# Optimization experiments

Measured on AMD Instinct MI355X. Metric: run time of the kernel, lower is better.

Reference implementation:

```python
import jax, jax.numpy as jnp
import numpy as np

NUM_HEADS = 12
HEAD_DIM = 64
HIDDEN = NUM_HEADS * HEAD_DIM


def setup_inputs() -> dict:
    key = jax.random.key(0)
    ks = jax.random.split(key, 10)
    B, S, N_ROT = 8, 1374, 1369
    s = 0.02
    return {
        "hidden_states": jax.random.normal(ks[0], (B, S, HIDDEN), jnp.float32),
        "sin": jax.random.normal(ks[1], (N_ROT, HEAD_DIM), jnp.float32),
        "cos": jax.random.normal(ks[2], (N_ROT, HEAD_DIM), jnp.float32),
        "Wq": jax.random.normal(ks[3], (HIDDEN, HIDDEN), jnp.float32) * s,
        "bq": jax.random.normal(ks[4], (HIDDEN,), jnp.float32) * s,
        "Wk": jax.random.normal(ks[5], (HIDDEN, HIDDEN), jnp.float32) * s,
        "Wv": jax.random.normal(ks[6], (HIDDEN, HIDDEN), jnp.float32) * s,
        "bv": jax.random.normal(ks[7], (HIDDEN,), jnp.float32) * s,
        "Wp": jax.random.normal(ks[8], (HIDDEN, HIDDEN), jnp.float32) * s,
        "bp": jax.random.normal(ks[9], (HIDDEN,), jnp.float32) * s,
    }


def _rotate_half(x):
    x1, x2 = jnp.split(x, 2, axis=-1)
    return jnp.concatenate([-x2, x1], axis=-1)


def _rope_apply(x, sin, cos):
    return x * cos + _rotate_half(x) * sin


def reference(hidden_states, sin, cos, Wq, bq, Wk, Wv, bv, Wp, bp):
    B, S, _ = hidden_states.shape
    scaling = HEAD_DIM ** -0.5

    def to_heads(x):  # [B,S,HIDDEN] -> [B,H,S,D]
        return x.reshape(B, S, NUM_HEADS, HEAD_DIM).transpose(0, 2, 1, 3)

    q = to_heads(hidden_states @ Wq.T + bq)
    k = to_heads(hidden_states @ Wk.T)  # no key bias (mask_k_bias)
    v = to_heads(hidden_states @ Wv.T + bv)

    # RoPE only on patch tokens (prefix = cls + register tokens untouched)
    prefix = S - sin.shape[-2]
    q = jnp.concatenate([q[:, :, :prefix], _rope_apply(q[:, :, prefix:], sin, cos)], axis=2)
    k = jnp.concatenate([k[:, :, :prefix], _rope_apply(k[:, :, prefix:], sin, cos)], axis=2)

    # eager attention: softmax in float32, no mask, no dropout (eval)
    scores = jnp.einsum("bhqd,bhkd->bhqk", q, k) * scaling
    probs = jax.nn.softmax(scores.astype(jnp.float32), axis=-1).astype(q.dtype)
    ctx = jnp.einsum("bhqk,bhkd->bqhd", probs, v).reshape(B, S, HIDDEN)
    return ctx @ Wp.T + bp
```

## Files before the change

### kernel.cpp

```cpp
#include <hip/hip_runtime.h>
#include <stdint.h>

typedef unsigned short u16;
typedef unsigned int u32;
typedef u16 u16x8 __attribute__((ext_vector_type(8)));
typedef __bf16 bf16x8 __attribute__((ext_vector_type(8)));
typedef float f32x4 __attribute__((ext_vector_type(4)));

#define S_LEN 1374
#define S_PAD 1408
#define PRE_TOK 5
#define HID 768
#define NH 12
#define MPAD 11008

__device__ __forceinline__ u16 f2bf(float f) {
    union { float f; u32 u; } v; v.f = f;
    u32 r = v.u + 0x7fffu + ((v.u >> 16) & 1u);
    return (u16)(r >> 16);
}
__device__ __forceinline__ bf16x8 as_bf(u16x8 v) { bf16x8 r; __builtin_memcpy(&r, &v, 16); return r; }
__device__ __forceinline__ bf16x8 lds_load8(const u16* p) {
    u16x8 t = *(const u16x8*)p;
    return as_bf(t);
}
__device__ __forceinline__ u32 cvtpk_bf16(float lo, float hi) {
    u32 r;
    asm("v_cvt_pk_bf16_f32 %0, %1, %2" : "=v"(r) : "v"(lo), "v"(hi));
    return r;
}
__device__ __forceinline__ float fexp2(float x) {
    float r;
    asm("v_exp_f32 %0, %1" : "=v"(r) : "v"(x));
    return r;
}
__device__ __forceinline__ void gload16(void* lds, const void* g) {
    unsigned int __attribute__((address_space(1)))* gp =
        (unsigned int __attribute__((address_space(1)))*)(unsigned long long)g;
    unsigned int __attribute__((address_space(3)))* lp =
        (unsigned int __attribute__((address_space(3)))*)(unsigned int)(unsigned long long)lds;
    __builtin_amdgcn_global_load_lds(gp, lp, 16, 0, 0);
}
__device__ __forceinline__ int xcd_swz(int orig, int nwg) {
    int qd = nwg >> 3, rd = nwg & 7;
    int xcd = orig & 7, rem = orig >> 3;
    return (xcd < rd ? xcd * (qd + 1) : rd * (qd + 1) + (xcd - rd) * qd) + rem;
}


__global__ __launch_bounds__(256) void pack_x(const float* __restrict__ X, u16* __restrict__ Xb) {
    size_t i = (size_t)blockIdx.x * 256 + threadIdx.x;
    size_t e = i * 8;
    const size_t TOT = (size_t)10992 * HID;
    u16x8 o = {0,0,0,0,0,0,0,0};
    if (e < TOT) {
        f32x4 a = *(const f32x4*)(X + e);
        f32x4 b = *(const f32x4*)(X + e + 4);
#pragma unroll
        for (int j = 0; j < 4; ++j) { o[j] = f2bf(a[j]); o[4 + j] = f2bf(b[j]); }
    }
    *(u16x8*)(Xb + e) = o;
}

__global__ __launch_bounds__(256) void pack_w(
    const float* __restrict__ Wq, const float* __restrict__ Wk, const float* __restrict__ Wv,
    const float* __restrict__ Wp, const float* __restrict__ bq, const float* __restrict__ bv,
    u16* __restrict__ wqkv, u16* __restrict__ wpb, float* __restrict__ bqkv)
{
    int g = blockIdx.x * 256 + threadIdx.x;
    const int QKV8 = 2304 * HID / 8;
    const int P8 = HID * HID / 8;
    if (g < QKV8) {
        int e = g * 8;
        int row = e / HID, col = e - row * HID;
        const float* src = (row < 768) ? (Wq + (size_t)row * HID + col)
                         : (row < 1536) ? (Wk + (size_t)(row - 768) * HID + col)
                                        : (Wv + (size_t)(row - 1536) * HID + col);
        u16x8 o;
#pragma unroll
        for (int j = 0; j < 8; ++j) o[j] = f2bf(src[j]);
        *(u16x8*)(wqkv + e) = o;
    } else if (g < QKV8 + P8) {
        int e = (g - QKV8) * 8;
        u16x8 o;
#pragma unroll
        for (int j = 0; j < 8; ++j) o[j] = f2bf(Wp[e + j]);
        *(u16x8*)(wpb + e) = o;
    }
    if (g < 288) {
        int e = g * 8;
#pragma unroll
        for (int j = 0; j < 8; ++j) {
            int c = e + j;
            bqkv[c] = (c < 768) ? bq[c] : (c < 1536 ? 0.f : bv[c - 1536]);
        }
    }
}


template <int EPI>
__global__ __launch_bounds__(256) void gemm_nt(
    const u16* __restrict__ A, const u16* __restrict__ B, const float* __restrict__ bias,
    float* __restrict__ Yf, u16* __restrict__ Qh, u16* __restrict__ Kh,
    u16* __restrict__ Yv, const float* __restrict__ SN, const float* __restrict__ CS,
    int N, int K, int nx, int nwg)
{
    __shared__ u16 As[128 * 64];
    __shared__ u16 Bs[128 * 64];
    int tid = threadIdx.x;
    int w = tid >> 6, l = tid & 63;
    int fr = l & 15, fg = l >> 4;
    int wg = xcd_swz(blockIdx.x, nwg);
    int col0 = (wg % nx) * 128;
    int row0 = (wg / nx) * 128;
    int wr = (w >> 1) * 64, wc = (w & 1) * 64;

    f32x4 zero4 = {0.f, 0.f, 0.f, 0.f};
    f32x4 acc[4][4];
#pragma unroll
    for (int m = 0; m < 4; ++m)
#pragma unroll
        for (int n = 0; n < 4; ++n) acc[m][n] = zero4;

    int srow[4], soff[4];
#pragma unroll
    for (int i = 0; i < 4; ++i) {
        int sbyte = (i * 4 + w) * 1024 + l * 16;
        int r = sbyte >> 7;
        int ir = (sbyte & 127) ^ ((r & 7) << 4);
        srow[i] = r; soff[i] = ir >> 1;
    }

    for (int kt = 0; kt < K; kt += 64) {
#pragma unroll
        for (int i = 0; i < 4; ++i) {
            int sb = (i * 4 + w) * 1024;
            gload16((char*)As + sb, A + (size_t)(row0 + srow[i]) * K + kt + soff[i]);
            gload16((char*)Bs + sb, B + (size_t)(col0 + srow[i]) * K + kt + soff[i]);
        }
        __syncthreads();
#pragma unroll
        for (int c = 0; c < 2; ++c) {
            bf16x8 af[4], bfr[4];
#pragma unroll
            for (int m = 0; m < 4; ++m) {
                int r = wr + m * 16 + fr;
                int byte_ = (c * 64 + fg * 16) ^ ((r & 7) << 4);
                af[m] = lds_load8(As + r * 64 + (byte_ >> 1));
            }
#pragma unroll
            for (int n = 0; n < 4; ++n) {
                int r = wc + n * 16 + fr;
                int byte_ = (c * 64 + fg * 16) ^ ((r & 7) << 4);
                bfr[n] = lds_load8(Bs + r * 64 + (byte_ >> 1));
            }
#pragma unroll
            for (int m = 0; m < 4; ++m)
#pragma unroll
                for (int n = 0; n < 4; ++n)
                    acc[m][n] = __builtin_amdgcn_mfma_f32_16x16x32_bf16(af[m], bfr[n], acc[m][n], 0, 0, 0);
        }
        __syncthreads();
    }

    if (EPI == 1) {
#pragma unroll
        for (int m = 0; m < 4; ++m)
#pragma unroll
            for (int n = 0; n < 4; ++n) {
                int gn = col0 + wc + n * 16 + fr;
                float bvv = bias[gn];
#pragma unroll
                for (int j = 0; j < 4; ++j) {
                    int gm = row0 + wr + m * 16 + fg * 4 + j;
                    if (gm < 10992) Yf[(size_t)gm * N + gn] = acc[m][n][j] + bvv;
                }
            }
    } else {
        int sect = col0 >= 1536 ? 2 : (col0 >= 768 ? 1 : 0);
        if (sect == 2) {
#pragma unroll
            for (int m = 0; m < 4; ++m)
#pragma unroll
                for (int n = 0; n < 4; ++n) {
                    int gn = col0 + wc + n * 16 + fr;
                    float bvv = bias[gn];
#pragma unroll
                    for (int j = 0; j < 4; ++j) {
                        int gm = row0 + wr + m * 16 + fg * 4 + j;
                        if (gm < 10992)
                            Yv[(size_t)gm * HID + (gn - 1536)] = f2bf(acc[m][n][j] + bvv);
                    }
                }
        } else {
            u16* H = sect ? Kh : Qh;
            const float QS = sect ? 1.f : 0.125f * 1.44269504088896f;
            int hh = ((col0 + wc) >> 6) - sect * NH;
            float bv4[4];
#pragma unroll
            for (int n = 0; n < 4; ++n) bv4[n] = bias[col0 + wc + n * 16 + fr];
#pragma unroll
            for (int m = 0; m < 4; ++m)
#pragma unroll
                for (int j = 0; j < 4; ++j) {
                    int gm = row0 + wr + m * 16 + fg * 4 + j;
                    if (gm < 10992) {
                        int b = gm / 1374, s = gm - b * 1374;
                        size_t ob = ((size_t)(b * NH + hh) * S_PAD + s) * 64;
#pragma unroll
                        for (int n2 = 0; n2 < 2; ++n2) {
                            int d = n2 * 16 + fr;
                            float v1 = acc[m][n2][j] + bv4[n2];
                            float v2 = acc[m][n2 + 2][j] + bv4[n2 + 2];
                            float a1 = v1, a2 = v2;
                            if (s >= PRE_TOK) {
                                size_t rr = (size_t)(s - PRE_TOK) * 64;
                                float c1 = CS[rr + d], s1 = SN[rr + d];
                                float c2 = CS[rr + d + 32], s2 = SN[rr + d + 32];
                                a1 = v1 * c1 - v2 * s1;
                                a2 = v2 * c2 + v1 * s2;
                            }
                            H[ob + d]      = f2bf(a1 * QS);
                            H[ob + d + 32] = f2bf(a2 * QS);
                        }
                    }
                }
        }
    }
}


__global__ __launch_bounds__(256) void v_pack(const u16* __restrict__ Yv, u16* __restrict__ Vt) {
    int st = blockIdx.x, bh = blockIdx.y;
    int b = bh / NH, h = bh - b * NH;
    int tid = threadIdx.x;
    int sl = tid >> 2, dg = (tid & 3) * 8;
    int s = st * 64 + sl;
    __shared__ u16 vtile[64 * 64];

    u16x8 a = {0,0,0,0,0,0,0,0}, a2 = {0,0,0,0,0,0,0,0};
    if (s < S_LEN) {
        size_t base = ((size_t)b * S_LEN + s) * HID + h * 64;
        a  = *(const u16x8*)(Yv + base + dg);
        a2 = *(const u16x8*)(Yv + base + 32 + dg);
    }
#pragma unroll
    for (int j = 0; j < 8; ++j) {
        vtile[(dg + j) * 64 + sl] = a[j];
        vtile[(32 + dg + j) * 64 + sl] = a2[j];
    }
    __syncthreads();
    int d = tid >> 2, so = (tid & 3) * 8;
    u16x8 ov0 = *(const u16x8*)(vtile + d * 64 + so);
    u16x8 ov1 = *(const u16x8*)(vtile + d * 64 + so + 32);
    size_t vrow = ((size_t)bh * 64 + d) * S_PAD + st * 64;
    *(u16x8*)(Vt + vrow + so) = ov0;
    *(u16x8*)(Vt + vrow + so + 32) = ov1;
}


#define FLASH_BODY(Kc, Vc, KsN, VsN, ktn, DO_STAGE, DO_MASK)                          \
    {                                                                                 \
        asm volatile("s_waitcnt vmcnt(0) lgkmcnt(0)" ::: "memory");                   \
        __syncthreads();                                                              \
        if (DO_STAGE) {                                                               \
            int k0n = (ktn) * 32;                                                     \
            gload16((char*)(KsN) + sb, Kb + (size_t)k0n * 64 + kfix);                 \
            gload16((char*)(VsN) + sb, Vb + (size_t)k0n + vfix);                      \
        }                                                                             \
        f32x4 sf[2];                                                                  \
        __builtin_amdgcn_s_setprio(1);                                                \
        _Pragma("unroll")                                                             \
        for (int n = 0; n < 2; ++n) {                                                 \
            f32x4 qk = zero4;                                                         \
            _Pragma("unroll")                                                         \
            for (int c = 0; c < 2; ++c) {                                             \
                int byte_ = (c * 64 + fg * 16) ^ ((fr & 7) << 4);                     \
                bf16x8 kf = lds_load8((Kc) + (n * 16 + fr) * 64 + (byte_ >> 1));      \
                qk = __builtin_amdgcn_mfma_f32_16x16x32_bf16(kf, qf[c], qk, 0, 0, 0); \
            }                                                                         \
            sf[n] = qk;                                                               \
        }                                                                             \
        __builtin_amdgcn_s_setprio(0);                                                \
        if (DO_MASK) {                                                                \
            _Pragma("unroll")                                                         \
            for (int n = 0; n < 2; ++n)                                               \
                _Pragma("unroll")                                                     \
                for (int j = 0; j < 4; ++j)                                           \
                    if (1344 + 8 * fg + 4 * n + j >= S_LEN) sf[n][j] = -1e30f;        \
        }                                                                             \
        _Pragma("unroll")                                                             \
        for (int n = 0; n < 2; ++n)                                                   \
            _Pragma("unroll")                                                         \
            for (int j = 0; j < 4; ++j) sf[n][j] = fexp2(sf[n][j]);                   \
        union PA { u32 w2[4]; bf16x8 v; } pa;                                         \
        pa.w2[0] = cvtpk_bf16(sf[0][0], sf[0][1]);                                    \
        pa.w2[1] = cvtpk_bf16(sf[0][2], sf[0][3]);                                    \
        pa.w2[2] = cvtpk_bf16(sf[1][0], sf[1][1]);                                    \
        pa.w2[3] = cvtpk_bf16(sf[1][2], sf[1][3]);                                    \
        __builtin_amdgcn_s_setprio(1);                                                \
        lsum = __builtin_amdgcn_mfma_f32_16x16x32_bf16(pa.v, ones, lsum, 0, 0, 0);    \
        _Pragma("unroll")                                                             \
        for (int nd = 0; nd < 4; ++nd) {                                              \
            int byte_ = ((nd >> 1) * 64 + fg * 16) ^ ((fr & 7) << 4);                 \
            bf16x8 vf = lds_load8((Vc) + ((nd & 1) * 16 + fr) * 64 + (byte_ >> 1));   \
            octx[nd] = __builtin_amdgcn_mfma_f32_16x16x32_bf16(pa.v, vf, octx[nd], 0, 0, 0); \
        }                                                                             \
        __builtin_amdgcn_s_setprio(0);                                                \
    }

__global__ __launch_bounds__(256, 8) void flash(
    const u16* __restrict__ Qh, const u16* __restrict__ Kh, const u16* __restrict__ Vt,
    u16* __restrict__ ctxO)
{
    int wg = (blockIdx.x & 7) * 264 + (blockIdx.x >> 3);
    int qt = wg % 22, bh = wg / 22;
    int b = bh / NH, h = bh - b * NH;
    int q0 = qt * 64;
    int tid = threadIdx.x, w = tid >> 6, l = tid & 63;
    int fr = l & 15, fg = l >> 4;

    __shared__ u16 Ks0[32 * 64], Ks1[32 * 64];
    __shared__ u16 Vs0[32 * 64], Vs1[32 * 64];

    const u16* Qb = Qh + (size_t)bh * S_PAD * 64;
    const u16* Kb = Kh + (size_t)bh * S_PAD * 64;
    const u16* Vb = Vt + (size_t)bh * 64 * S_PAD;

    bf16x8 qf[2];
    {
        int qrow = q0 + w * 16 + fr;
#pragma unroll
        for (int c = 0; c < 2; ++c)
            qf[c] = as_bf(*(const u16x8*)(Qb + (size_t)qrow * 64 + c * 32 + fg * 8));
    }

    u16x8 ones_u = {0x3F80, 0x3F80, 0x3F80, 0x3F80, 0x3F80, 0x3F80, 0x3F80, 0x3F80};
    bf16x8 ones = as_bf(ones_u);

    f32x4 zero4 = {0.f, 0.f, 0.f, 0.f};
    f32x4 octx[4] = {zero4, zero4, zero4, zero4};
    f32x4 lsum = zero4;

    int r = w * 8 + (l >> 3);
    int bb = (l & 7) * 16;
    int ir = bb ^ ((r & 7) << 4);
    int gk = ((r >> 2) & 3) * 8 + ((r >> 4) & 1) * 4 + (r & 3);
    int kfix = gk * 64 + (ir >> 1);
    int vfix = (r + (ir >> 6) * 32) * S_PAD + ((ir & 63) >> 1);
    int sb = w * 1024;

    gload16((char*)Ks0 + sb, Kb + kfix);
    gload16((char*)Vs0 + sb, Vb + vfix);

    for (int kt = 0; kt < 42; kt += 2) {
        FLASH_BODY(Ks0, Vs0, Ks1, Vs1, kt + 1, true, false);
        FLASH_BODY(Ks1, Vs1, Ks0, Vs0, kt + 2, true, false);
    }
    FLASH_BODY(Ks0, Vs0, Ks1, Vs1, 0, false, true);

#pragma unroll
    for (int j = 0; j < 4; ++j) {
        int q = q0 + w * 16 + fg * 4 + j;
        if (q < S_LEN) {
            float inv = 1.f / lsum[j];
            size_t rowb = ((size_t)b * S_LEN + q) * HID + h * 64;
#pragma unroll
            for (int nd = 0; nd < 4; ++nd)
                ctxO[rowb + nd * 16 + fr] = f2bf(octx[nd][j] * inv);
        }
    }
}


extern "C" void kernel_launch(void* const* d_in, const int* in_sizes, int n_in,
                              void* d_out, int out_size, void* d_ws, size_t ws_size,
                              hipStream_t stream) {
    (void)in_sizes; (void)n_in; (void)out_size; (void)ws_size;
    const float* X  = (const float*)d_in[0];
    const float* SN = (const float*)d_in[1];
    const float* CS = (const float*)d_in[2];
    const float* Wq = (const float*)d_in[3];
    const float* bq = (const float*)d_in[4];
    const float* Wk = (const float*)d_in[5];
    const float* Wv = (const float*)d_in[6];
    const float* bv = (const float*)d_in[7];
    const float* Wp = (const float*)d_in[8];
    const float* bp = (const float*)d_in[9];
    float* OUT = (float*)d_out;
    char* ws = (char*)d_ws;

    u16*   xb   = (u16*)(ws);
    u16*   wqkv = (u16*)(ws + 16908288);
    u16*   wpb  = (u16*)(ws + 20447232);
    float* bqkv = (float*)(ws + 21626880);
    u16*   Yv   = (u16*)(ws + 21636096);
    u16*   Qh   = (u16*)(ws + 72360960);
    u16*   Kh   = (u16*)(ws + 89662464);
    u16*   Vt   = (u16*)(ws + 106963968);
    u16*   ctx  = xb;

    pack_x<<<4128, 256, 0, stream>>>(X, xb);
    pack_w<<<1152, 256, 0, stream>>>(Wq, Wk, Wv, Wp, bq, bv, wqkv, wpb, bqkv);
    gemm_nt<2><<<1548, 256, 0, stream>>>(xb, wqkv, bqkv, nullptr, Qh, Kh, Yv, SN, CS, 2304, 768, 18, 1548);
    v_pack<<<dim3(22, 96), 256, 0, stream>>>(Yv, Vt);
    flash<<<2112, 256, 0, stream>>>(Qh, Kh, Vt, ctx);
    gemm_nt<1><<<516, 256, 0, stream>>>(ctx, wpb, bp, OUT, nullptr, nullptr, nullptr, nullptr, nullptr, 768, 768, 6, 516);
}
```

Before: 189.2 us.

## Double-buffer LDS tiles in GEMM to overlap global loads with MFMA

```diff
diff --git a/kernel.cpp b/kernel.cpp
--- a/kernel.cpp
+++ b/kernel.cpp
@@ -98,6 +98,44 @@
 }
 
 
+#define GSTAGE(AA, BB, kk)                                                             \
+    {                                                                                  \
+        _Pragma("unroll")                                                              \
+        for (int i = 0; i < 4; ++i) {                                                  \
+            int sb = (i * 4 + w) * 1024;                                               \
+            gload16((char*)(AA) + sb, A + (size_t)(row0 + srow[i]) * K + (kk) + soff[i]); \
+            gload16((char*)(BB) + sb, B + (size_t)(col0 + srow[i]) * K + (kk) + soff[i]); \
+        }                                                                              \
+    }
+
+#define GBODY(CA, CB, NA, NB, ktn, DO_STAGE)                                           \
+    {                                                                                  \
+        asm volatile("s_waitcnt vmcnt(0) lgkmcnt(0)" ::: "memory");                    \
+        __syncthreads();                                                               \
+        if (DO_STAGE) GSTAGE(NA, NB, ktn);                                             \
+        _Pragma("unroll")                                                              \
+        for (int c = 0; c < 2; ++c) {                                                  \
+            bf16x8 af[4], bfr[4];                                                      \
+            _Pragma("unroll")                                                          \
+            for (int m = 0; m < 4; ++m) {                                              \
+                int r = wr + m * 16 + fr;                                              \
+                int byte_ = (c * 64 + fg * 16) ^ ((r & 7) << 4);                       \
+                af[m] = lds_load8((CA) + r * 64 + (byte_ >> 1));                       \
+            }                                                                          \
+            _Pragma("unroll")                                                          \
+            for (int n = 0; n < 4; ++n) {                                              \
+                int r = wc + n * 16 + fr;                                              \
+                int byte_ = (c * 64 + fg * 16) ^ ((r & 7) << 4);                       \
+                bfr[n] = lds_load8((CB) + r * 64 + (byte_ >> 1));                      \
+            }                                                                          \
+            _Pragma("unroll")                                                          \
+            for (int m = 0; m < 4; ++m)                                                \
+                _Pragma("unroll")                                                      \
+                for (int n = 0; n < 4; ++n)                                            \
+                    acc[m][n] = __builtin_amdgcn_mfma_f32_16x16x32_bf16(af[m], bfr[n], acc[m][n], 0, 0, 0); \
+        }                                                                              \
+    }
+
 template <int EPI>
 __global__ __launch_bounds__(256) void gemm_nt(
     const u16* __restrict__ A, const u16* __restrict__ B, const float* __restrict__ bias,
@@ -105,8 +143,8 @@
     u16* __restrict__ Yv, const float* __restrict__ SN, const float* __restrict__ CS,
     int N, int K, int nx, int nwg)
 {
-    __shared__ u16 As[128 * 64];
-    __shared__ u16 Bs[128 * 64];
+    __shared__ u16 As0[128 * 64], Bs0[128 * 64];
+    __shared__ u16 As1[128 * 64], Bs1[128 * 64];
     int tid = threadIdx.x;
     int w = tid >> 6, l = tid & 63;
     int fr = l & 15, fg = l >> 4;
@@ -131,36 +169,10 @@
         srow[i] = r; soff[i] = ir >> 1;
     }
 
-    for (int kt = 0; kt < K; kt += 64) {
-#pragma unroll
-        for (int i = 0; i < 4; ++i) {
-            int sb = (i * 4 + w) * 1024;
-            gload16((char*)As + sb, A + (size_t)(row0 + srow[i]) * K + kt + soff[i]);
-            gload16((char*)Bs + sb, B + (size_t)(col0 + srow[i]) * K + kt + soff[i]);
-        }
-        __syncthreads();
-#pragma unroll
-        for (int c = 0; c < 2; ++c) {
-            bf16x8 af[4], bfr[4];
-#pragma unroll
-            for (int m = 0; m < 4; ++m) {
-                int r = wr + m * 16 + fr;
-                int byte_ = (c * 64 + fg * 16) ^ ((r & 7) << 4);
-                af[m] = lds_load8(As + r * 64 + (byte_ >> 1));
-            }
-#pragma unroll
-            for (int n = 0; n < 4; ++n) {
-                int r = wc + n * 16 + fr;
-                int byte_ = (c * 64 + fg * 16) ^ ((r & 7) << 4);
-                bfr[n] = lds_load8(Bs + r * 64 + (byte_ >> 1));
-            }
-#pragma unroll
-            for (int m = 0; m < 4; ++m)
-#pragma unroll
-                for (int n = 0; n < 4; ++n)
-                    acc[m][n] = __builtin_amdgcn_mfma_f32_16x16x32_bf16(af[m], bfr[n], acc[m][n], 0, 0, 0);
-        }
-        __syncthreads();
+    GSTAGE(As0, Bs0, 0);
+    for (int kt = 0; kt < K; kt += 128) {
+        GBODY(As0, Bs0, As1, Bs1, kt + 64, true);
+        GBODY(As1, Bs1, As0, Bs0, kt + 128, kt + 128 < K);
     }
 
     if (EPI == 1) {
```

Result: slower. 200.6 us (+6.0%).

## Process two 16-row query sub-tiles per wave in flash attention

Applied to the files above, without the earlier changes.

```diff
diff --git a/kernel.cpp b/kernel.cpp
--- a/kernel.cpp
+++ b/kernel.cpp
@@ -268,18 +268,19 @@
             gload16((char*)(KsN) + sb, Kb + (size_t)k0n * 64 + kfix);                 \
             gload16((char*)(VsN) + sb, Vb + (size_t)k0n + vfix);                      \
         }                                                                             \
-        f32x4 sf[2];                                                                  \
+        f32x4 sf[2][2];                                                               \
         __builtin_amdgcn_s_setprio(1);                                                \
         _Pragma("unroll")                                                             \
         for (int n = 0; n < 2; ++n) {                                                 \
-            f32x4 qk = zero4;                                                         \
+            f32x4 q0a = zero4, q1a = zero4;                                           \
             _Pragma("unroll")                                                         \
             for (int c = 0; c < 2; ++c) {                                             \
                 int byte_ = (c * 64 + fg * 16) ^ ((fr & 7) << 4);                     \
                 bf16x8 kf = lds_load8((Kc) + (n * 16 + fr) * 64 + (byte_ >> 1));      \
-                qk = __builtin_amdgcn_mfma_f32_16x16x32_bf16(kf, qf[c], qk, 0, 0, 0); \
+                q0a = __builtin_amdgcn_mfma_f32_16x16x32_bf16(kf, qf[0][c], q0a, 0, 0, 0); \
+                q1a = __builtin_amdgcn_mfma_f32_16x16x32_bf16(kf, qf[1][c], q1a, 0, 0, 0); \
             }                                                                         \
-            sf[n] = qk;                                                               \
+            sf[0][n] = q0a; sf[1][n] = q1a;                                           \
         }                                                                             \
         __builtin_amdgcn_s_setprio(0);                                                \
         if (DO_MASK) {                                                                \
@@ -287,36 +288,43 @@
             for (int n = 0; n < 2; ++n)                                               \
                 _Pragma("unroll")                                                     \
                 for (int j = 0; j < 4; ++j)                                           \
-                    if (1344 + 8 * fg + 4 * n + j >= S_LEN) sf[n][j] = -1e30f;        \
+                    if (1344 + 8 * fg + 4 * n + j >= S_LEN) {                         \
+                        sf[0][n][j] = -1e30f; sf[1][n][j] = -1e30f;                   \
+                    }                                                                 \
         }                                                                             \
+        union PA { u32 w2[4]; bf16x8 v; } pa[2];                                      \
         _Pragma("unroll")                                                             \
-        for (int n = 0; n < 2; ++n)                                                   \
+        for (int qq = 0; qq < 2; ++qq) {                                              \
             _Pragma("unroll")                                                         \
-            for (int j = 0; j < 4; ++j) sf[n][j] = fexp2(sf[n][j]);                   \
-        union PA { u32 w2[4]; bf16x8 v; } pa;                                         \
-        pa.w2[0] = cvtpk_bf16(sf[0][0], sf[0][1]);                                    \
-        pa.w2[1] = cvtpk_bf16(sf[0][2], sf[0][3]);                                    \
-        pa.w2[2] = cvtpk_bf16(sf[1][0], sf[1][1]);                                    \
-        pa.w2[3] = cvtpk_bf16(sf[1][2], sf[1][3]);                                    \
+            for (int n = 0; n < 2; ++n)                                               \
+                _Pragma("unroll")                                                     \
+                for (int j = 0; j < 4; ++j) sf[qq][n][j] = fexp2(sf[qq][n][j]);       \
+            pa[qq].w2[0] = cvtpk_bf16(sf[qq][0][0], sf[qq][0][1]);                    \
+            pa[qq].w2[1] = cvtpk_bf16(sf[qq][0][2], sf[qq][0][3]);                    \
+            pa[qq].w2[2] = cvtpk_bf16(sf[qq][1][0], sf[qq][1][1]);                    \
+            pa[qq].w2[3] = cvtpk_bf16(sf[qq][1][2], sf[qq][1][3]);                    \
+        }                                                                             \
         __builtin_amdgcn_s_setprio(1);                                                \
-        lsum = __builtin_amdgcn_mfma_f32_16x16x32_bf16(pa.v, ones, lsum, 0, 0, 0);    \
+        lsum0 = __builtin_amdgcn_mfma_f32_16x16x32_bf16(pa[0].v, ones, lsum0, 0, 0, 0); \
+        lsum1 = __builtin_amdgcn_mfma_f32_16x16x32_bf16(pa[1].v, ones, lsum1, 0, 0, 0); \
         _Pragma("unroll")                                                             \
         for (int nd = 0; nd < 4; ++nd) {                                              \
             int byte_ = ((nd >> 1) * 64 + fg * 16) ^ ((fr & 7) << 4);                 \
             bf16x8 vf = lds_load8((Vc) + ((nd & 1) * 16 + fr) * 64 + (byte_ >> 1));   \
-            octx[nd] = __builtin_amdgcn_mfma_f32_16x16x32_bf16(pa.v, vf, octx[nd], 0, 0, 0); \
+            octx[0][nd] = __builtin_amdgcn_mfma_f32_16x16x32_bf16(pa[0].v, vf, octx[0][nd], 0, 0, 0); \
+            octx[1][nd] = __builtin_amdgcn_mfma_f32_16x16x32_bf16(pa[1].v, vf, octx[1][nd], 0, 0, 0); \
         }                                                                             \
         __builtin_amdgcn_s_setprio(0);                                                \
     }
 
-__global__ __launch_bounds__(256, 8) void flash(
+__global__ __launch_bounds__(256, 4) void flash(
     const u16* __restrict__ Qh, const u16* __restrict__ Kh, const u16* __restrict__ Vt,
     u16* __restrict__ ctxO)
 {
-    int wg = (blockIdx.x & 7) * 264 + (blockIdx.x >> 3);
-    int qt = wg % 22, bh = wg / 22;
+    int wg = (blockIdx.x & 7) * 132 + (blockIdx.x >> 3);
+    int qt = wg % 11, bh = wg / 11;
     int b = bh / NH, h = bh - b * NH;
-    int q0 = qt * 64;
+    int q0 = qt * 128;
     int tid = threadIdx.x, w = tid >> 6, l = tid & 63;
     int fr = l & 15, fg = l >> 4;
 
@@ -327,20 +335,25 @@
     const u16* Kb = Kh + (size_t)bh * S_PAD * 64;
     const u16* Vb = Vt + (size_t)bh * 64 * S_PAD;
 
-    bf16x8 qf[2];
-    {
-        int qrow = q0 + w * 16 + fr;
+    bf16x8 qf[2][2];
+#pragma unroll
+    for (int qq = 0; qq < 2; ++qq) {
+        int qrow = q0 + w * 32 + qq * 16 + fr;
 #pragma unroll
         for (int c = 0; c < 2; ++c)
-            qf[c] = as_bf(*(const u16x8*)(Qb + (size_t)qrow * 64 + c * 32 + fg * 8));
+            qf[qq][c] = as_bf(*(const u16x8*)(Qb + (size_t)qrow * 64 + c * 32 + fg * 8));
     }
 
     u16x8 ones_u = {0x3F80, 0x3F80, 0x3F80, 0x3F80, 0x3F80, 0x3F80, 0x3F80, 0x3F80};
     bf16x8 ones = as_bf(ones_u);
 
     f32x4 zero4 = {0.f, 0.f, 0.f, 0.f};
-    f32x4 octx[4] = {zero4, zero4, zero4, zero4};
-    f32x4 lsum = zero4;
+    f32x4 octx[2][4];
+#pragma unroll
+    for (int qq = 0; qq < 2; ++qq)
+#pragma unroll
+        for (int nd = 0; nd < 4; ++nd) octx[qq][nd] = zero4;
+    f32x4 lsum0 = zero4, lsum1 = zero4;
 
     int r = w * 8 + (l >> 3);
     int bb = (l & 7) * 16;
@@ -360,16 +373,19 @@
     FLASH_BODY(Ks0, Vs0, Ks1, Vs1, 0, false, true);
 
 #pragma unroll
-    for (int j = 0; j < 4; ++j) {
-        int q = q0 + w * 16 + fg * 4 + j;
-        if (q < S_LEN) {
-            float inv = 1.f / lsum[j];
-            size_t rowb = ((size_t)b * S_LEN + q) * HID + h * 64;
-#pragma unroll
-            for (int nd = 0; nd < 4; ++nd)
-                ctxO[rowb + nd * 16 + fr] = f2bf(octx[nd][j] * inv);
+    for (int qq = 0; qq < 2; ++qq)
+#pragma unroll
+        for (int j = 0; j < 4; ++j) {
+            int q = q0 + w * 32 + qq * 16 + fg * 4 + j;
+            if (q < S_LEN) {
+                float lv = qq ? lsum1[j] : lsum0[j];
+                float inv = 1.f / lv;
+                size_t rowb = ((size_t)b * S_LEN + q) * HID + h * 64;
+#pragma unroll
+                for (int nd = 0; nd < 4; ++nd)
+                    ctxO[rowb + nd * 16 + fr] = f2bf(octx[qq][nd][j] * inv);
+            }
         }
-    }
 }
 
 
@@ -404,6 +420,6 @@
     pack_w<<<1152, 256, 0, stream>>>(Wq, Wk, Wv, Wp, bq, bv, wqkv, wpb, bqkv);
     gemm_nt<2><<<1548, 256, 0, stream>>>(xb, wqkv, bqkv, nullptr, Qh, Kh, Yv, SN, CS, 2304, 768, 18, 1548);
     v_pack<<<dim3(22, 96), 256, 0, stream>>>(Yv, Vt);
-    flash<<<2112, 256, 0, stream>>>(Qh, Kh, Vt, ctx);
+    flash<<<1056, 256, 0, stream>>>(Qh, Kh, Vt, ctx);
     gemm_nt<1><<<516, 256, 0, stream>>>(ctx, wpb, bp, OUT, nullptr, nullptr, nullptr, nullptr, nullptr, 768, 768, 6, 516);
 }
```

After: 183.4 us. -3.1%, faster.
